# Kernel optimization log

Hardware: AMD Instinct MI355X
Metric: run time of the kernel (lower is better)

## Reference

```python
import jax, jax.numpy as jnp
from jax import lax
import numpy as np

NPOINT = 1024
RADIUS = 0.25
NSAMPLE = 32
USE_XYZ = True


def setup_inputs() -> dict:
    key = jax.random.key(0)
    k1, k2 = jax.random.split(key)
    xyz = jax.random.normal(k1, (8, 8192, 3), dtype=jnp.float32)
    points = jax.random.normal(k2, (8, 8192, 32), dtype=jnp.float32)
    return {"xyz": xyz, "points": points}


def furthest_point_sample(xyz, npoint):
    """Iterative FPS; returns (B, npoint, 3) sampled coordinates.
    Matches torch reference: seeded with xyz[:, 0], squared-distance metric."""
    B, N, _ = xyz.shape
    first = xyz[:, 0]  # (B, 3)
    d0 = jnp.full((B, N), 1e38, dtype=xyz.dtype)

    def step(carry, _):
        dist, last = carry  # dist: (B,N), last: (B,3)
        d2 = jnp.sum((xyz - last[:, None, :]) ** 2, axis=-1)  # (B,N)
        dist = jnp.minimum(dist, d2)
        idx = jnp.argmax(dist, axis=1)  # (B,)
        nxt = jnp.take_along_axis(xyz, idx[:, None, None], axis=1)[:, 0]  # (B,3)
        return (dist, nxt), nxt

    _, outs = lax.scan(step, (d0, first), None, length=npoint - 1)  # (npoint-1, B, 3)
    return jnp.concatenate([first[None], outs], axis=0).transpose(1, 0, 2)  # (B,npoint,3)


def ball_query(radius, nsample, xyz, new_xyz):
    """First `nsample` indices within `radius` of each center (ascending index
    order), padded with the first found index — matches pointnet2 CUDA kernel.
    Returns (B, npoint, nsample) int32."""
    N = xyz.shape[1]
    d2 = jnp.sum((new_xyz[:, :, None, :] - xyz[:, None, :, :]) ** 2, axis=-1)  # (B,npoint,N)
    mask = d2 < radius * radius
    ar = jnp.arange(N, dtype=jnp.int32)
    # top_k on negated indices -> smallest valid indices first
    score = jnp.where(mask, -ar, jnp.int32(-(N + 1)))
    vals, _ = lax.top_k(score, nsample)  # (B,npoint,nsample), descending
    valid = vals > -(N + 1)
    idx = jnp.where(valid, -vals, -vals[..., :1])  # pad with first hit
    return idx.astype(jnp.int32)


def group_points(points, idx):
    """points (B,N,C), idx (B,npoint,nsample) -> (B,npoint,nsample,C)."""
    B, npoint, nsample = idx.shape
    C = points.shape[-1]
    flat = idx.reshape(B, npoint * nsample)  # (B, npoint*nsample)
    g = jnp.take_along_axis(points, flat[:, :, None], axis=1)
    return g.reshape(B, npoint, nsample, C)


def reference(xyz, points):
    new_xyz = furthest_point_sample(xyz, NPOINT)  # (B,npoint,3)
    idx = ball_query(RADIUS, NSAMPLE, xyz, new_xyz)  # (B,npoint,nsample)
    grouped_xyz = group_points(xyz, idx) - new_xyz[:, :, None, :]  # center-relative
    grouped_points = group_points(points, idx)
    if USE_XYZ:
        new_points = jnp.concatenate([grouped_xyz, grouped_points], axis=-1)
    else:
        new_points = grouped_points
    return new_xyz, new_points
```

## Files before the change

kernel.cpp:

```cpp
#include <hip/hip_runtime.h>

#define BATCH   8
#define NPTS    8192
#define NPOINT  1024
#define NSAMPLE 32
#define CHANC   32
#define OUTC    35
#define R2      0.0625f

#define NBLK    256
#define NTHR    512
#define NJOBS   (BATCH * NPOINT / 2)

typedef float v2f __attribute__((ext_vector_type(2)));
typedef unsigned long long u64;
typedef unsigned int u32;

template <int CTRL>
__device__ __forceinline__ float dpp_max_step(float v) {
    int r = __builtin_amdgcn_update_dpp(__float_as_int(v), __float_as_int(v),
                                        CTRL, 0xf, 0xf, false);
    return fmaxf(v, __int_as_float(r));
}
#define DPP_ROW_SHR(n)  (0x110 | (n))
#define DPP_BCAST15     0x142
#define DPP_BCAST31     0x143

__device__ __forceinline__ u64 u64max(u64 a, u64 b) { return a > b ? a : b; }

__device__ __forceinline__ void barrier_lds_only() {
    asm volatile("s_waitcnt lgkmcnt(0)\n\ts_barrier" ::: "memory");
}

__global__ __launch_bounds__(NTHR) void fused_kernel(
        const float* __restrict__ xyz,
        const float* __restrict__ points,
        float* __restrict__ new_xyz,
        float* __restrict__ out,
        u64* __restrict__ slots,
        u32* __restrict__ counter)
{
#pragma clang fp contract(off)
    __shared__ float4 pts[NPTS];
    __shared__ u64 partial[2][8];
    __shared__ int qidx[2][4][NSAMPLE];
    __shared__ int qcnt[2][4];
    __shared__ int jobsh;

    const int blk  = blockIdx.x;
    const int t    = threadIdx.x;
    const int lane = t & 63;

    if (blk < BATCH) {
        const int b = blk;
        const int w = t >> 6;
        const float* bx = xyz + (size_t)b * NPTS * 3;
        u64* bslot = slots + (size_t)b * NPOINT * 3;
        float* oxyz = new_xyz + (size_t)b * NPOINT * 3;

        v2f px[8], py[8], pz[8], dist[8];
        {
            float f[48];
            float4* fq = (float4*)f;
            const float4* s4 = (const float4*)bx + t * 12;
#pragma unroll
            for (int q = 0; q < 12; ++q) fq[q] = s4[q];
#pragma unroll
            for (int p = 0; p < 8; ++p) {
                px[p] = (v2f){f[6 * p + 0], f[6 * p + 3]};
                py[p] = (v2f){f[6 * p + 1], f[6 * p + 4]};
                pz[p] = (v2f){f[6 * p + 2], f[6 * p + 5]};
                dist[p] = (v2f){1e38f, 1e38f};
            }
#pragma unroll
            for (int i = 0; i < 16; ++i) {
                const int j  = t * 16 + i;
                const int js = j ^ ((j >> 4) & 7);
                pts[js] = make_float4(f[3 * i + 0], f[3 * i + 1], f[3 * i + 2], 0.0f);
            }
        }
        __syncthreads();

        float4 c0 = pts[0];
        float lx = c0.x, ly = c0.y, lz = c0.z;
        if (t < 3) {
            const float c = (t == 0) ? lx : (t == 1) ? ly : lz;
            const u64 tag = (u64)(u32)(b * NPOINT + 1);
            __hip_atomic_store(&bslot[t], (tag << 32) | (u64)__float_as_uint(c),
                               __ATOMIC_RELAXED, __HIP_MEMORY_SCOPE_AGENT);
            oxyz[t] = c;
        }

        for (int s = 1; s < NPOINT; ++s) {
            const v2f lx2 = (v2f){lx, lx};
            const v2f ly2 = (v2f){ly, ly};
            const v2f lz2 = (v2f){lz, lz};
            float bestv = -1.0f;
            int   bi    = 0;
#pragma unroll
            for (int p = 0; p < 8; ++p) {
                const v2f dx = px[p] - lx2;
                const v2f dy = py[p] - ly2;
                const v2f dz = pz[p] - lz2;
                const v2f d2 = (dx * dx + dy * dy) + dz * dz;
                const float d0 = fminf(dist[p].x, d2.x);
                const float d1 = fminf(dist[p].y, d2.y);
                dist[p] = (v2f){d0, d1};
                if (d0 > bestv) { bestv = d0; bi = 2 * p; }
                if (d1 > bestv) { bestv = d1; bi = 2 * p + 1; }
            }
            const int besti = (t << 4) + bi;

            float v = bestv;
            v = dpp_max_step<DPP_ROW_SHR(1)>(v);
            v = dpp_max_step<DPP_ROW_SHR(2)>(v);
            v = dpp_max_step<DPP_ROW_SHR(4)>(v);
            v = dpp_max_step<DPP_ROW_SHR(8)>(v);
            v = dpp_max_step<DPP_BCAST15>(v);
            v = dpp_max_step<DPP_BCAST31>(v);
            const float smax = __int_as_float(__builtin_amdgcn_readlane(__float_as_int(v), 63));

            const u64 m   = __ballot(bestv == smax);
            const int par = s & 1;
            if (lane == (int)__builtin_ctzll(m)) {
                partial[par][w] = ((u64)__float_as_uint(smax) << 32)
                                  | (unsigned)(~besti);
            }
            barrier_lds_only();

            const u64* P = partial[par];
            const u64 a0 = P[0], a1 = P[1], a2 = P[2], a3 = P[3];
            const u64 a4 = P[4], a5 = P[5], a6 = P[6], a7 = P[7];
            const u64 bp =
                u64max(u64max(u64max(a0, a1), u64max(a2, a3)),
                       u64max(u64max(a4, a5), u64max(a6, a7)));
            const int idx = (int)(~(unsigned)bp);
            const int js  = idx ^ ((idx >> 4) & 7);
            const float4 cw = pts[js];
            lx = cw.x; ly = cw.y; lz = cw.z;
            if (t < 3) {
                const float c = (t == 0) ? lx : (t == 1) ? ly : lz;
                const u64 tag = (u64)(u32)(b * NPOINT + s + 1);
                __hip_atomic_store(&bslot[3 * s + t],
                                   (tag << 32) | (u64)__float_as_uint(c),
                                   __ATOMIC_RELAXED, __HIP_MEMORY_SCOPE_AGENT);
                oxyz[3 * s + t] = c;
            }
        }
    } else {
        for (;;) {
            if (t == 0) jobsh = (int)atomicAdd(counter, 1u);
            __syncthreads();
            const int job = jobsh;
            if (job >= NJOBS) break;

            const int half = t >> 8;
            const int gw   = job * 2 + half;
            const int bb   = gw >> 10;
            const int r    = (t >> 6) & 3;

            const u32 tag = (u32)(gw + 1);
            u64* sl = slots + (size_t)gw * 3;
            u64 w0, w1, w2;
            for (;;) {
                w0 = __hip_atomic_load(&sl[0], __ATOMIC_RELAXED, __HIP_MEMORY_SCOPE_AGENT);
                w1 = __hip_atomic_load(&sl[1], __ATOMIC_RELAXED, __HIP_MEMORY_SCOPE_AGENT);
                w2 = __hip_atomic_load(&sl[2], __ATOMIC_RELAXED, __HIP_MEMORY_SCOPE_AGENT);
                if ((u32)(w0 >> 32) == tag && (u32)(w1 >> 32) == tag &&
                    (u32)(w2 >> 32) == tag) break;
                __builtin_amdgcn_s_sleep(32);
            }
            const float cx = __uint_as_float((u32)w0);
            const float cy = __uint_as_float((u32)w1);
            const float cz = __uint_as_float((u32)w2);

            const float* bxr = xyz + (size_t)bb * NPTS * 3;
            int k = 0;
            const int qbase = r << 11;
            for (int base = qbase; base < qbase + 2048; base += 256) {
                float qx[4], qy[4], qz[4];
#pragma unroll
                for (int u = 0; u < 4; ++u) {
                    const int j = base + u * 64 + lane;
                    qx[u] = bxr[3 * j + 0];
                    qy[u] = bxr[3 * j + 1];
                    qz[u] = bxr[3 * j + 2];
                }
                bool in[4];
#pragma unroll
                for (int u = 0; u < 4; ++u) {
                    const float dx = qx[u] - cx;
                    const float dy = qy[u] - cy;
                    const float dz = qz[u] - cz;
                    const float d2 = (dx * dx + dy * dy) + dz * dz;
                    in[u] = d2 < R2;
                }
#pragma unroll
                for (int u = 0; u < 4; ++u) {
                    const u64 mu = __ballot(in[u]);
                    const int pre = __popcll(mu & ((1ull << lane) - 1ull));
                    if (in[u] && (k + pre) < NSAMPLE) qidx[half][r][k + pre] = base + u * 64 + lane;
                    k += __popcll(mu);
                }
                if (k >= NSAMPLE) break;
            }
            if (k > NSAMPLE) k = NSAMPLE;
            if (lane == 0) qcnt[half][r] = k;
            __syncthreads();

            const int c0n = qcnt[half][0], c1n = qcnt[half][1];
            const int c2n = qcnt[half][2], c3n = qcnt[half][3];
            const int o1 = c0n, o2 = c0n + c1n, o3 = o2 + c2n;
            const int total = o3 + c3n;
            const int kk = total < NSAMPLE ? total : NSAMPLE;
            const int rq = (c0n > 0) ? 0 : (c1n > 0) ? 1 : (c2n > 0) ? 2 : 3;
            const int firstIdx = qidx[half][rq][0];

            float*       o    = out + (size_t)gw * NSAMPLE * OUTC;
            const float* prow = points + (size_t)bb * NPTS * CHANC;
            const int t256 = t & 255;
            for (int e = t256; e < NSAMPLE * OUTC; e += 256) {
                const int sI = e / OUTC;
                const int c  = e - sI * OUTC;
                int j;
                if (sI < kk) {
                    const int rr  = (int)(sI >= o1) + (int)(sI >= o2) + (int)(sI >= o3);
                    const int off = (rr == 0) ? 0 : (rr == 1) ? o1 : (rr == 2) ? o2 : o3;
                    j = qidx[half][rr][sI - off];
                } else {
                    j = firstIdx;
                }
                float v;
                if (c < 3) {
                    const float pv = bxr[3 * j + c];
                    const float cc = (c == 0) ? cx : (c == 1) ? cy : cz;
                    v = pv - cc;
                } else {
                    v = prow[j * CHANC + (c - 3)];
                }
                o[e] = v;
            }
        }
    }
}

extern "C" void kernel_launch(void* const* d_in, const int* in_sizes, int n_in,
                              void* d_out, int out_size, void* d_ws, size_t ws_size,
                              hipStream_t stream) {
    const float* xyz    = (const float*)d_in[0];
    const float* points = (const float*)d_in[1];
    float* new_xyz    = (float*)d_out;
    float* new_points = new_xyz + (size_t)BATCH * NPOINT * 3;

    u64* slots   = (u64*)d_ws;
    u32* counter = (u32*)((char*)d_ws + (size_t)BATCH * NPOINT * 3 * sizeof(u64));

    hipMemsetAsync(d_ws, 0, (size_t)BATCH * NPOINT * 3 * sizeof(u64) + 64, stream);

    fused_kernel<<<NBLK, NTHR, 0, stream>>>(xyz, points, new_xyz, new_points,
                                            slots, counter);
}
```

Baseline: 982.9 us.

## Replace atomic job counter with static strided scheduling and single-wave slot polling

Worker blocks now take center pairs in a fixed strided order instead of pulling jobs from a global atomic counter. One wavefront polls the six slot words with a ballot and writes the centers to shared memory, so the other waves no longer spin on global memory. The grid drops from 256 to 128 blocks. This removes the atomic contention and the redundant polling traffic that competes with the FPS blocks, but fewer worker blocks and static assignment may leave the grouping work less parallel or worse balanced.

Result: slower. 1.106 ms (+12.5%).

```diff
diff --git a/kernel.cpp b/kernel.cpp
--- a/kernel.cpp
+++ b/kernel.cpp
@@ -8,9 +8,9 @@
 #define OUTC    35
 #define R2      0.0625f
 
-#define NBLK    256
-#define NTHR    512
-#define NJOBS   (BATCH * NPOINT / 2)
+#define NBLK    128
+#define NW      (NBLK - BATCH)
+#define NCTR    (BATCH * NPOINT)
 
 typedef float v2f __attribute__((ext_vector_type(2)));
 typedef unsigned long long u64;
@@ -32,20 +32,19 @@
     asm volatile("s_waitcnt lgkmcnt(0)\n\ts_barrier" ::: "memory");
 }
 
-__global__ __launch_bounds__(NTHR) void fused_kernel(
+__global__ __launch_bounds__(512) void fused_kernel(
         const float* __restrict__ xyz,
         const float* __restrict__ points,
         float* __restrict__ new_xyz,
         float* __restrict__ out,
-        u64* __restrict__ slots,
-        u32* __restrict__ counter)
+        u64* __restrict__ slots)
 {
 #pragma clang fp contract(off)
     __shared__ float4 pts[NPTS];
     __shared__ u64 partial[2][8];
     __shared__ int qidx[2][4][NSAMPLE];
     __shared__ int qcnt[2][4];
-    __shared__ int jobsh;
+    __shared__ float ccsh[6];
 
     const int blk  = blockIdx.x;
     const int t    = threadIdx.x;
@@ -148,31 +147,32 @@
             }
         }
     } else {
-        for (;;) {
-            if (t == 0) jobsh = (int)atomicAdd(counter, 1u);
+        const int wb = blk - BATCH;
+        for (int g0 = wb * 2; g0 < NCTR; g0 += NW * 2) {
+            if ((t >> 6) == 0) {
+                const int  gwl  = g0 + (lane >= 3 ? 1 : 0);
+                u64* sl  = (lane < 6) ? slots + (size_t)gwl * 3 + (lane % 3)
+                                      : slots;
+                const u32 tagl = (lane < 6) ? (u32)(gwl + 1) : 0u;
+                u64 rv;
+                for (;;) {
+                    rv = __hip_atomic_load(sl, __ATOMIC_RELAXED,
+                                           __HIP_MEMORY_SCOPE_AGENT);
+                    const bool ready = (lane >= 6) | ((u32)(rv >> 32) == tagl);
+                    if (__ballot(ready) == ~0ull) break;
+                    __builtin_amdgcn_s_sleep(64);
+                }
+                if (lane < 6) ccsh[lane] = __uint_as_float((u32)rv);
+            }
             __syncthreads();
-            const int job = jobsh;
-            if (job >= NJOBS) break;
 
             const int half = t >> 8;
-            const int gw   = job * 2 + half;
+            const int gw   = g0 + half;
             const int bb   = gw >> 10;
             const int r    = (t >> 6) & 3;
-
-            const u32 tag = (u32)(gw + 1);
-            u64* sl = slots + (size_t)gw * 3;
-            u64 w0, w1, w2;
-            for (;;) {
-                w0 = __hip_atomic_load(&sl[0], __ATOMIC_RELAXED, __HIP_MEMORY_SCOPE_AGENT);
-                w1 = __hip_atomic_load(&sl[1], __ATOMIC_RELAXED, __HIP_MEMORY_SCOPE_AGENT);
-                w2 = __hip_atomic_load(&sl[2], __ATOMIC_RELAXED, __HIP_MEMORY_SCOPE_AGENT);
-                if ((u32)(w0 >> 32) == tag && (u32)(w1 >> 32) == tag &&
-                    (u32)(w2 >> 32) == tag) break;
-                __builtin_amdgcn_s_sleep(32);
-            }
-            const float cx = __uint_as_float((u32)w0);
-            const float cy = __uint_as_float((u32)w1);
-            const float cz = __uint_as_float((u32)w2);
+            const float cx = ccsh[half * 3 + 0];
+            const float cy = ccsh[half * 3 + 1];
+            const float cz = ccsh[half * 3 + 2];
 
             const float* bxr = xyz + (size_t)bb * NPTS * 3;
             int k = 0;
@@ -252,11 +252,10 @@
     float* new_xyz    = (float*)d_out;
     float* new_points = new_xyz + (size_t)BATCH * NPOINT * 3;
 
-    u64* slots   = (u64*)d_ws;
-    u32* counter = (u32*)((char*)d_ws + (size_t)BATCH * NPOINT * 3 * sizeof(u64));
-
-    hipMemsetAsync(d_ws, 0, (size_t)BATCH * NPOINT * 3 * sizeof(u64) + 64, stream);
-
-    fused_kernel<<<NBLK, NTHR, 0, stream>>>(xyz, points, new_xyz, new_points,
-                                            slots, counter);
-}
+    u64* slots = (u64*)d_ws;
+
+    hipMemsetAsync(slots, 0, (size_t)NCTR * 3 * sizeof(u64), stream);
+
+    fused_kernel<<<NBLK, 512, 0, stream>>>(xyz, points, new_xyz, new_points,
+                                           slots);
+}
```
